# Kernel optimization log

Measured on AMD Instinct MI355X. Metric: run time of the kernel, lower is better.

## Reference

```python
import jax, jax.numpy as jnp
import numpy as np
from math import sqrt

D_MODEL = 1024
N_HEADS = 16
E = D_MODEL // N_HEADS  # d_keys = d_values = 64


def setup_inputs() -> dict:
    key = jax.random.key(0)
    ks = jax.random.split(key, 11)
    B, L, S = 2, 2048, 2048
    s = 1.0 / sqrt(D_MODEL)
    return {
        "queries": jax.random.normal(ks[0], (B, L, D_MODEL), jnp.float32),
        "keys": jax.random.normal(ks[1], (B, S, D_MODEL), jnp.float32),
        "values": jax.random.normal(ks[2], (B, S, D_MODEL), jnp.float32),
        "Wq": jax.random.normal(ks[3], (D_MODEL, D_MODEL), jnp.float32) * s,
        "bq": jnp.zeros((D_MODEL,), jnp.float32),
        "Wk": jax.random.normal(ks[4], (D_MODEL, D_MODEL), jnp.float32) * s,
        "bk": jnp.zeros((D_MODEL,), jnp.float32),
        "Wv": jax.random.normal(ks[5], (D_MODEL, D_MODEL), jnp.float32) * s,
        "bv": jnp.zeros((D_MODEL,), jnp.float32),
        "Wo": jax.random.normal(ks[6], (D_MODEL, D_MODEL), jnp.float32) * s,
        "bo": jnp.zeros((D_MODEL,), jnp.float32),
    }


def reference(queries, keys, values, Wq, bq, Wk, bk, Wv, bv, Wo, bo):
    B, L, _ = queries.shape
    S = keys.shape[1]
    H = N_HEADS
    # projections -> [B, L/S, H, E]
    q = (queries @ Wq + bq).reshape(B, L, H, E)
    k = (keys @ Wk + bk).reshape(B, S, H, E)
    v = (values @ Wv + bv).reshape(B, S, H, E)
    scale = 1.0 / sqrt(E)
    scores = jnp.einsum('blhe,bshe->bhls', q, k)  # [B,H,L,S]
    A = jax.nn.softmax(scale * scores, axis=-1)   # dropout = identity (eval)
    V = jnp.einsum('bhls,bshd->blhd', A, v)       # [B,L,H,E]
    out = V.reshape(B, L, H * E) @ Wo + bo
    return out
```

## Files before the change

### kernel.cpp

```cpp
#include <hip/hip_runtime.h>
#include <hip/hip_bf16.h>
#include <stdint.h>

#define BATCH 2
#define SEQ   2048
#define DM    1024
#define NH    16
#define EH    64
#define MROWS (BATCH*SEQ)

typedef __attribute__((ext_vector_type(8))) short  short8;
typedef __attribute__((ext_vector_type(4))) float  floatx4;
typedef __attribute__((ext_vector_type(8))) unsigned short ushort8v;
typedef __attribute__((ext_vector_type(4))) unsigned short ushort4v;

__device__ __forceinline__ unsigned short f2bf(float f) {
    return (unsigned short)((__float_as_uint(f) + 0x8000u) >> 16);
}

__device__ __forceinline__ void gload_lds16(const void* g, void* l) {
    __builtin_amdgcn_global_load_lds(
        (const __attribute__((address_space(1))) unsigned int*)g,
        (__attribute__((address_space(3))) unsigned int*)l, 16, 0, 0);
}

__global__ __launch_bounds__(256)
void transpose_w(const float* __restrict__ W0, const float* __restrict__ W1,
                 const float* __restrict__ W2, const float* __restrict__ W3,
                 unsigned short* __restrict__ T0, unsigned short* __restrict__ T1,
                 unsigned short* __restrict__ T2, unsigned short* __restrict__ T3,
                 int zbase)
{
    int z = zbase + blockIdx.z;
    const float* W = (z == 0) ? W0 : (z == 1) ? W1 : (z == 2) ? W2 : W3;
    unsigned short* T = (z == 0) ? T0 : (z == 1) ? T1 : (z == 2) ? T2 : T3;
    __shared__ float t[32][33];
    const int tid = threadIdx.x;
    const int k0 = blockIdx.y * 32, n0 = blockIdx.x * 32;
    {
        int r = tid >> 3, c4 = (tid & 7) * 4;
        float4 u = *(const float4*)&W[(size_t)(k0 + r) * DM + n0 + c4];
        t[r][c4 + 0] = u.x; t[r][c4 + 1] = u.y; t[r][c4 + 2] = u.z; t[r][c4 + 3] = u.w;
    }
    __syncthreads();
    {
        int n = tid >> 3, k4 = (tid & 7) * 4;
        ushort4v o;
        o[0] = f2bf(t[k4 + 0][n]); o[1] = f2bf(t[k4 + 1][n]);
        o[2] = f2bf(t[k4 + 2][n]); o[3] = f2bf(t[k4 + 3][n]);
        *(ushort4v*)&T[(size_t)(n0 + n) * DM + k0 + k4] = o;
    }
}

struct ProjArgs {
    const float* act[3];
    const unsigned short* wt[3];
    const float* bias[3];
    unsigned short* C[3];
    float oscale[3];
};

__global__ __launch_bounds__(256)
void proj_qkv(ProjArgs pa)
{
    const int z = blockIdx.z;
    const bool vt = (z == 2);
    const int linear = (int)(blockIdx.x + gridDim.x * blockIdx.y);
    int rb, cb;
    if (!vt) { rb = linear & 31; cb = linear >> 5; }
    else     { cb = linear & 31; rb = linear >> 5; }
    const int row0 = rb * 128, col0 = cb * 128;

    const float* act = pa.act[z];
    const unsigned short* wt = pa.wt[z];
    const int actBase = vt ? col0 : row0;
    const int wtBase  = vt ? row0 : col0;

    __shared__ unsigned short As[128 * 32];
    __shared__ unsigned short Bs[128 * 32];
    unsigned short* convDst  = vt ? Bs : As;
    unsigned short* asyncDst = vt ? As : Bs;

    const int tid = threadIdx.x;
    const int lane = tid & 63, w = tid >> 6;
    const int lane15 = lane & 15, quad = lane >> 4;

    floatx4 acc[2][8] = {};

    float4 pre[4];
    {
        const float* p0 = &act[(size_t)(actBase + (tid >> 2)) * DM + ((tid & 3) * 8)];
        const float* p1 = &act[(size_t)(actBase + ((256 + tid) >> 2)) * DM + ((tid & 3) * 8)];
        pre[0] = *(const float4*)p0; pre[1] = *(const float4*)(p0 + 4);
        pre[2] = *(const float4*)p1; pre[3] = *(const float4*)(p1 + 4);
    }

    for (int kt = 0; kt < DM; kt += 32) {
        __syncthreads();
#pragma unroll
        for (int rr = 0; rr < 2; ++rr) {
            int c = rr * 256 + tid;
            ushort8v o8;
            float4 u0 = pre[rr * 2], u1 = pre[rr * 2 + 1];
            o8[0] = f2bf(u0.x); o8[1] = f2bf(u0.y); o8[2] = f2bf(u0.z); o8[3] = f2bf(u0.w);
            o8[4] = f2bf(u1.x); o8[5] = f2bf(u1.y); o8[6] = f2bf(u1.z); o8[7] = f2bf(u1.w);
            *(ushort8v*)&convDst[(size_t)c * 8] = o8;
        }
#pragma unroll
        for (int rr = 0; rr < 2; ++rr) {
            int c = rr * 256 + w * 64 + lane;
            int row = c >> 2, kel = (c & 3) * 8;
            gload_lds16(&wt[(size_t)(wtBase + row) * DM + kt + kel],
                        (char*)asyncDst + (size_t)(rr * 256 + w * 64) * 16);
        }
        __syncthreads();

        if (kt + 32 < DM) {
            int kn = kt + 32;
            const float* p0 = &act[(size_t)(actBase + (tid >> 2)) * DM + kn + ((tid & 3) * 8)];
            const float* p1 = &act[(size_t)(actBase + ((256 + tid) >> 2)) * DM + kn + ((tid & 3) * 8)];
            pre[0] = *(const float4*)p0; pre[1] = *(const float4*)(p0 + 4);
            pre[2] = *(const float4*)p1; pre[3] = *(const float4*)(p1 + 4);
        }

        short8 af[2], bf[8];
#pragma unroll
        for (int i = 0; i < 2; ++i)
            af[i] = *(const short8*)&As[(w * 32 + i * 16 + lane15) * 32 + quad * 8];
#pragma unroll
        for (int j = 0; j < 8; ++j)
            bf[j] = *(const short8*)&Bs[(j * 16 + lane15) * 32 + quad * 8];
#pragma unroll
        for (int i = 0; i < 2; ++i)
#pragma unroll
            for (int j = 0; j < 8; ++j)
                acc[i][j] = __builtin_amdgcn_mfma_f32_16x16x32_bf16(af[i], bf[j], acc[i][j], 0, 0, 0);
    }

    const float* bias = pa.bias[z];
    const float os = pa.oscale[z];
    unsigned short* C = pa.C[z];
#pragma unroll
    for (int i = 0; i < 2; ++i) {
#pragma unroll
        for (int j = 0; j < 8; ++j) {
#pragma unroll
            for (int r = 0; r < 4; ++r) {
                int row = row0 + w * 32 + i * 16 + quad * 4 + r;
                int col = col0 + j * 16 + lane15;
                if (!vt) {
                    float v = (acc[i][j][r] + bias[col]) * os;
                    int b = row >> 11, l = row & (SEQ - 1);
                    int h = col >> 6,  e = col & (EH - 1);
                    C[((size_t)(b * NH + h) * SEQ + l) * EH + e] = f2bf(v);
                } else {
                    float v = acc[i][j][r] + bias[row];
                    int h = row >> 6,  e = row & (EH - 1);
                    int b = col >> 11, l = col & (SEQ - 1);
                    C[((size_t)(b * NH + h) * EH + e) * SEQ + l] = f2bf(v);
                }
            }
        }
    }
}

__global__ __launch_bounds__(256)
void gemm_out(const unsigned short* __restrict__ ctx,
              const unsigned short* __restrict__ WoT,
              const float* __restrict__ bo,
              float* __restrict__ out)
{
    const int linear = (int)(blockIdx.x + gridDim.x * blockIdx.y);
    const int rb = linear & 31, cb = linear >> 5;
    const int row0 = rb * 128, col0 = cb * 64;

    __shared__ unsigned short As[128 * 32];
    __shared__ unsigned short Bs[64 * 32];

    const int tid = threadIdx.x;
    const int lane = tid & 63, w = tid >> 6;
    const int lane15 = lane & 15, quad = lane >> 4;

    floatx4 acc[2][4] = {};

    for (int kt = 0; kt < DM; kt += 32) {
        __syncthreads();
#pragma unroll
        for (int rr = 0; rr < 2; ++rr) {
            int c = rr * 256 + w * 64 + lane;
            int row = c >> 2, kel = (c & 3) * 8;
            gload_lds16(&ctx[(size_t)(row0 + row) * DM + kt + kel],
                        (char*)As + (size_t)(rr * 256 + w * 64) * 16);
        }
        {
            int c = w * 64 + lane;
            int row = c >> 2, kel = (c & 3) * 8;
            gload_lds16(&WoT[(size_t)(col0 + row) * DM + kt + kel],
                        (char*)Bs + (size_t)(w * 64) * 16);
        }
        __syncthreads();

        short8 af[2], bf[4];
#pragma unroll
        for (int i = 0; i < 2; ++i)
            af[i] = *(const short8*)&As[(w * 32 + i * 16 + lane15) * 32 + quad * 8];
#pragma unroll
        for (int j = 0; j < 4; ++j)
            bf[j] = *(const short8*)&Bs[(j * 16 + lane15) * 32 + quad * 8];
#pragma unroll
        for (int i = 0; i < 2; ++i)
#pragma unroll
            for (int j = 0; j < 4; ++j)
                acc[i][j] = __builtin_amdgcn_mfma_f32_16x16x32_bf16(af[i], bf[j], acc[i][j], 0, 0, 0);
    }

#pragma unroll
    for (int i = 0; i < 2; ++i)
#pragma unroll
        for (int j = 0; j < 4; ++j)
#pragma unroll
            for (int r = 0; r < 4; ++r) {
                int row = row0 + w * 32 + i * 16 + quad * 4 + r;
                int col = col0 + j * 16 + lane15;
                out[(size_t)row * DM + col] = acc[i][j][r] + bo[col];
            }
}

__device__ __forceinline__ void stage_kv(const unsigned short* __restrict__ Kp,
                                         const unsigned short* __restrict__ Vp,
                                         int st, unsigned short* ksb, unsigned short* vsb,
                                         int w, int lane)
{
#pragma unroll
    for (int rr = 0; rr < 2; ++rr) {
        int p = rr * 256 + w * 64 + lane;
        int row = p >> 3;
        int gch = (p & 7) ^ (row & 7);
        gload_lds16(&Kp[(size_t)(st + row) * EH + gch * 8],
                    ksb + (size_t)(rr * 256 + w * 64) * 8);
        gload_lds16(&Vp[(size_t)row * SEQ + st + gch * 8],
                    vsb + (size_t)(rr * 256 + w * 64) * 8);
    }
}

__global__ __launch_bounds__(256)
void attn_mfma(const unsigned short* __restrict__ Qh,
               const unsigned short* __restrict__ Kh,
               const unsigned short* __restrict__ Vt,
               unsigned short* __restrict__ ctx)
{
    __shared__ unsigned short Ks[2][64 * 64];
    __shared__ unsigned short Vs[2][64 * 64];
    __shared__ unsigned short Ps[128][72];

    const int tid = threadIdx.x;
    const int lane = tid & 63, w = tid >> 6;
    const int lane15 = lane & 15, quad = lane >> 4;

    const int linear = (int)(blockIdx.x + 16 * (blockIdx.y + 16 * blockIdx.z));
    const int bhid = linear & 31;
    const int qt = linear >> 5;
    const int h = bhid & 15, b = bhid >> 4;

    const size_t bh = (size_t)(b * NH + h);
    const unsigned short* Kp = Kh + bh * SEQ * EH;
    const unsigned short* Vp = Vt + bh * EH * SEQ;

    short8 qf[2][2];
    {
        const unsigned short* Qp =
            Qh + (bh * SEQ + (size_t)qt * 128 + w * 32 + lane15) * EH;
#pragma unroll
        for (int ks = 0; ks < 2; ++ks) {
            qf[0][ks] = *(const short8*)(Qp + ks * 32 + quad * 8);
            qf[1][ks] = *(const short8*)(Qp + 16 * EH + ks * 32 + quad * 8);
        }
    }
    short8 ones;
#pragma unroll
    for (int i = 0; i < 8; ++i) ones[i] = (short)0x3F80;

    floatx4 o[2][4] = {};
    floatx4 lacc[2] = {};

    stage_kv(Kp, Vp, 0, Ks[0], Vs[0], w, lane);
    __syncthreads();
    int cur = 0;

    for (int st = 0; st < SEQ; st += 64) {
        int nxt = cur ^ 1;
        if (st + 64 < SEQ)
            stage_kv(Kp, Vp, st + 64, Ks[nxt], Vs[nxt], w, lane);
        const unsigned short* ksb = Ks[cur];
        const unsigned short* vsb = Vs[cur];

        floatx4 sacc[4][2] = {};
#pragma unroll
        for (int ts = 0; ts < 4; ++ts) {
#pragma unroll
            for (int ks = 0; ks < 2; ++ks) {
                short8 kf = *(const short8*)&ksb[((ts * 16 + lane15) << 6) +
                                                 ((((ks << 2) + quad) ^ (lane15 & 7)) << 3)];
                sacc[ts][0] = __builtin_amdgcn_mfma_f32_16x16x32_bf16(kf, qf[0][ks], sacc[ts][0], 0, 0, 0);
                sacc[ts][1] = __builtin_amdgcn_mfma_f32_16x16x32_bf16(kf, qf[1][ks], sacc[ts][1], 0, 0, 0);
            }
        }

#pragma unroll
        for (int ts = 0; ts < 4; ++ts)
#pragma unroll
            for (int nq = 0; nq < 2; ++nq) {
                unsigned int u0 = __float_as_uint(__builtin_amdgcn_exp2f(sacc[ts][nq][0])) + 0x8000u;
                unsigned int u1 = __float_as_uint(__builtin_amdgcn_exp2f(sacc[ts][nq][1])) + 0x8000u;
                unsigned int u2 = __float_as_uint(__builtin_amdgcn_exp2f(sacc[ts][nq][2])) + 0x8000u;
                unsigned int u3 = __float_as_uint(__builtin_amdgcn_exp2f(sacc[ts][nq][3])) + 0x8000u;
                uint2 pk;
                pk.x = (u0 >> 16) | (u1 & 0xFFFF0000u);
                pk.y = (u2 >> 16) | (u3 & 0xFFFF0000u);
                *(uint2*)&Ps[w * 32 + nq * 16 + lane15][ts * 16 + quad * 4] = pk;
            }

#pragma unroll
        for (int ks = 0; ks < 2; ++ks) {
            short8 pf[2];
#pragma unroll
            for (int mt = 0; mt < 2; ++mt) {
                pf[mt] = *(const short8*)&Ps[w * 32 + mt * 16 + lane15][ks * 32 + quad * 8];
                lacc[mt] = __builtin_amdgcn_mfma_f32_16x16x32_bf16(pf[mt], ones, lacc[mt], 0, 0, 0);
            }
#pragma unroll
            for (int t2 = 0; t2 < 4; ++t2) {
                short8 vf = *(const short8*)&vsb[((t2 * 16 + lane15) << 6) +
                                                 ((((ks << 2) + quad) ^ (lane15 & 7)) << 3)];
                o[0][t2] = __builtin_amdgcn_mfma_f32_16x16x32_bf16(pf[0], vf, o[0][t2], 0, 0, 0);
                o[1][t2] = __builtin_amdgcn_mfma_f32_16x16x32_bf16(pf[1], vf, o[1][t2], 0, 0, 0);
            }
        }
        __syncthreads();
        cur = nxt;
    }

#pragma unroll
    for (int mt = 0; mt < 2; ++mt) {
        float inv[4];
#pragma unroll
        for (int r = 0; r < 4; ++r) inv[r] = 1.0f / lacc[mt][r];
#pragma unroll
        for (int t2 = 0; t2 < 4; ++t2)
#pragma unroll
            for (int r = 0; r < 4; ++r) {
                int q = qt * 128 + w * 32 + mt * 16 + quad * 4 + r;
                int col = h * EH + t2 * 16 + lane15;
                ctx[((size_t)(b * SEQ + q)) * DM + col] = f2bf(o[mt][t2][r] * inv[r]);
            }
    }
}

extern "C" void kernel_launch(void* const* d_in, const int* in_sizes, int n_in,
                              void* d_out, int out_size, void* d_ws, size_t ws_size,
                              hipStream_t stream)
{
    const float* queries = (const float*)d_in[0];
    const float* keys    = (const float*)d_in[1];
    const float* values  = (const float*)d_in[2];
    const float* Wq = (const float*)d_in[3];
    const float* bq = (const float*)d_in[4];
    const float* Wk = (const float*)d_in[5];
    const float* bk = (const float*)d_in[6];
    const float* Wv = (const float*)d_in[7];
    const float* bv = (const float*)d_in[8];
    const float* Wo = (const float*)d_in[9];
    const float* bo = (const float*)d_in[10];
    float* out = (float*)d_out;

    unsigned short* ws = (unsigned short*)d_ws;
    const size_t MAT = (size_t)MROWS * DM;
    const size_t WSZ = (size_t)DM * DM;
    unsigned short* Qhp = ws;
    unsigned short* Khp = ws + MAT;
    unsigned short* Vtp = ws + 2 * MAT;
    unsigned short* ctx = ws + 3 * MAT;
    unsigned short* WqT = ctx;
    unsigned short* WkT = ctx + WSZ;
    unsigned short* WvT = ctx + 2 * WSZ;
    unsigned short* WoT = ws;

    const float qscale = 0.125f * 1.44269504088896f;

    transpose_w<<<dim3(DM / 32, DM / 32, 3), 256, 0, stream>>>(
        Wq, Wk, Wv, Wo, WqT, WkT, WvT, WoT, 0);

    ProjArgs pa;
    pa.act[0] = queries; pa.act[1] = keys; pa.act[2] = values;
    pa.wt[0] = WqT;      pa.wt[1] = WkT;   pa.wt[2] = WvT;
    pa.bias[0] = bq;     pa.bias[1] = bk;  pa.bias[2] = bv;
    pa.C[0] = Qhp;       pa.C[1] = Khp;    pa.C[2] = Vtp;
    pa.oscale[0] = qscale; pa.oscale[1] = 1.f; pa.oscale[2] = 1.f;
    proj_qkv<<<dim3(8, 32, 3), 256, 0, stream>>>(pa);

    attn_mfma<<<dim3(SEQ / 128, NH, BATCH), 256, 0, stream>>>(Qhp, Khp, Vtp, ctx);

    transpose_w<<<dim3(DM / 32, DM / 32, 1), 256, 0, stream>>>(
        Wq, Wk, Wv, Wo, WqT, WkT, WvT, WoT, 3);

    gemm_out<<<dim3(16, 32), 256, 0, stream>>>(ctx, WoT, bo, out);
}
```

Before: 227.4 us.

## Double-buffer LDS in projection GEMMs with XOR swizzle and 2x2 warp tiling

Both projection and output GEMMs now use two LDS buffers, prefetching the next K tile while computing the current one, so each iteration needs one barrier instead of two. LDS chunk positions are XOR-swizzled on store and load to reduce bank conflicts on the fragment reads. In the QKV projection, warps are rearranged into a 2x2 grid of 64x64 tiles, which cuts redundant B-fragment LDS reads. This doubles LDS use per block and may lower occupancy.

```diff
diff --git a/kernel.cpp b/kernel.cpp
--- a/kernel.cpp
+++ b/kernel.cpp
@@ -76,78 +76,94 @@
     const int actBase = vt ? col0 : row0;
     const int wtBase  = vt ? row0 : col0;
 
-    __shared__ unsigned short As[128 * 32];
-    __shared__ unsigned short Bs[128 * 32];
-    unsigned short* convDst  = vt ? Bs : As;
-    unsigned short* asyncDst = vt ? As : Bs;
+    __shared__ unsigned short As[2][128 * 32];
+    __shared__ unsigned short Bs[2][128 * 32];
+    unsigned short* conv[2] = { vt ? Bs[0] : As[0], vt ? Bs[1] : As[1] };
+    unsigned short* wdst[2] = { vt ? As[0] : Bs[0], vt ? As[1] : Bs[1] };
 
     const int tid = threadIdx.x;
     const int lane = tid & 63, w = tid >> 6;
     const int lane15 = lane & 15, quad = lane >> 4;
-
-    floatx4 acc[2][8] = {};
+    const int wr = (w >> 1) * 64, wc = (w & 1) * 64;
+
+    floatx4 acc[4][4] = {};
 
     float4 pre[4];
-    {
-        const float* p0 = &act[(size_t)(actBase + (tid >> 2)) * DM + ((tid & 3) * 8)];
-        const float* p1 = &act[(size_t)(actBase + ((256 + tid) >> 2)) * DM + ((tid & 3) * 8)];
+    const int arow = tid >> 2;
+    const int acol = (tid & 3) * 8;
+
+    auto loadPre = [&](int kt) {
+        const float* p0 = &act[(size_t)(actBase + arow) * DM + kt + acol];
+        const float* p1 = &act[(size_t)(actBase + 64 + arow) * DM + kt + acol];
         pre[0] = *(const float4*)p0; pre[1] = *(const float4*)(p0 + 4);
         pre[2] = *(const float4*)p1; pre[3] = *(const float4*)(p1 + 4);
-    }
-
-    for (int kt = 0; kt < DM; kt += 32) {
-        __syncthreads();
+    };
+    auto cvtStore = [&](unsigned short* dst) {
 #pragma unroll
         for (int rr = 0; rr < 2; ++rr) {
-            int c = rr * 256 + tid;
+            int row = rr * 64 + arow;
+            int cp = (tid & 3) ^ ((row >> 1) & 3);
+            float4 u0 = pre[rr * 2], u1 = pre[rr * 2 + 1];
             ushort8v o8;
-            float4 u0 = pre[rr * 2], u1 = pre[rr * 2 + 1];
             o8[0] = f2bf(u0.x); o8[1] = f2bf(u0.y); o8[2] = f2bf(u0.z); o8[3] = f2bf(u0.w);
             o8[4] = f2bf(u1.x); o8[5] = f2bf(u1.y); o8[6] = f2bf(u1.z); o8[7] = f2bf(u1.w);
-            *(ushort8v*)&convDst[(size_t)c * 8] = o8;
-        }
+            *(ushort8v*)&dst[(size_t)(row * 4 + cp) * 8] = o8;
+        }
+    };
+    auto stageW = [&](int kt, unsigned short* dst) {
 #pragma unroll
         for (int rr = 0; rr < 2; ++rr) {
-            int c = rr * 256 + w * 64 + lane;
-            int row = c >> 2, kel = (c & 3) * 8;
-            gload_lds16(&wt[(size_t)(wtBase + row) * DM + kt + kel],
-                        (char*)asyncDst + (size_t)(rr * 256 + w * 64) * 16);
-        }
+            int p = rr * 256 + w * 64 + lane;
+            int row = p >> 2;
+            int gch = (p & 3) ^ ((row >> 1) & 3);
+            gload_lds16(&wt[(size_t)(wtBase + row) * DM + kt + gch * 8],
+                        (char*)dst + (size_t)(rr * 256 + w * 64) * 16);
+        }
+    };
+
+    loadPre(0);
+    stageW(0, wdst[0]);
+    cvtStore(conv[0]);
+    loadPre(32);
+    __syncthreads();
+
+    const int sw = (lane15 >> 1) & 3;
+    for (int kt = 0; kt < DM; kt += 32) {
+        const int cur = (kt >> 5) & 1, nxt = cur ^ 1;
+        if (kt + 32 < DM) {
+            stageW(kt + 32, wdst[nxt]);
+            cvtStore(conv[nxt]);
+            if (kt + 64 < DM) loadPre(kt + 64);
+        }
+
+        const unsigned short* as = As[cur];
+        const unsigned short* bs = Bs[cur];
+        short8 af[4], bf[4];
+#pragma unroll
+        for (int i = 0; i < 4; ++i)
+            af[i] = *(const short8*)&as[(size_t)(wr + i * 16 + lane15) * 32 + ((quad ^ sw) << 3)];
+#pragma unroll
+        for (int j = 0; j < 4; ++j)
+            bf[j] = *(const short8*)&bs[(size_t)(wc + j * 16 + lane15) * 32 + ((quad ^ sw) << 3)];
+#pragma unroll
+        for (int i = 0; i < 4; ++i)
+#pragma unroll
+            for (int j = 0; j < 4; ++j)
+                acc[i][j] = __builtin_amdgcn_mfma_f32_16x16x32_bf16(af[i], bf[j], acc[i][j], 0, 0, 0);
         __syncthreads();
-
-        if (kt + 32 < DM) {
-            int kn = kt + 32;
-            const float* p0 = &act[(size_t)(actBase + (tid >> 2)) * DM + kn + ((tid & 3) * 8)];
-            const float* p1 = &act[(size_t)(actBase + ((256 + tid) >> 2)) * DM + kn + ((tid & 3) * 8)];
-            pre[0] = *(const float4*)p0; pre[1] = *(const float4*)(p0 + 4);
-            pre[2] = *(const float4*)p1; pre[3] = *(const float4*)(p1 + 4);
-        }
-
-        short8 af[2], bf[8];
-#pragma unroll
-        for (int i = 0; i < 2; ++i)
-            af[i] = *(const short8*)&As[(w * 32 + i * 16 + lane15) * 32 + quad * 8];
-#pragma unroll
-        for (int j = 0; j < 8; ++j)
-            bf[j] = *(const short8*)&Bs[(j * 16 + lane15) * 32 + quad * 8];
-#pragma unroll
-        for (int i = 0; i < 2; ++i)
-#pragma unroll
-            for (int j = 0; j < 8; ++j)
-                acc[i][j] = __builtin_amdgcn_mfma_f32_16x16x32_bf16(af[i], bf[j], acc[i][j], 0, 0, 0);
     }
 
     const float* bias = pa.bias[z];
     const float os = pa.oscale[z];
     unsigned short* C = pa.C[z];
 #pragma unroll
-    for (int i = 0; i < 2; ++i) {
-#pragma unroll
-        for (int j = 0; j < 8; ++j) {
+    for (int i = 0; i < 4; ++i) {
+#pragma unroll
+        for (int j = 0; j < 4; ++j) {
 #pragma unroll
             for (int r = 0; r < 4; ++r) {
-                int row = row0 + w * 32 + i * 16 + quad * 4 + r;
-                int col = col0 + j * 16 + lane15;
+                int row = row0 + wr + i * 16 + quad * 4 + r;
+                int col = col0 + wc + j * 16 + lane15;
                 if (!vt) {
                     float v = (acc[i][j][r] + bias[col]) * os;
                     int b = row >> 11, l = row & (SEQ - 1);
@@ -174,8 +190,8 @@
     const int rb = linear & 31, cb = linear >> 5;
     const int row0 = rb * 128, col0 = cb * 64;
 
-    __shared__ unsigned short As[128 * 32];
-    __shared__ unsigned short Bs[64 * 32];
+    __shared__ unsigned short As[2][128 * 32];
+    __shared__ unsigned short Bs[2][64 * 32];
 
     const int tid = threadIdx.x;
     const int lane = tid & 63, w = tid >> 6;
@@ -183,35 +199,51 @@
 
     floatx4 acc[2][4] = {};
 
+    auto stageA = [&](int kt, unsigned short* dst) {
+#pragma unroll
+        for (int rr = 0; rr < 2; ++rr) {
+            int p = rr * 256 + w * 64 + lane;
+            int row = p >> 2;
+            int gch = (p & 3) ^ ((row >> 1) & 3);
+            gload_lds16(&ctx[(size_t)(row0 + row) * DM + kt + gch * 8],
+                        (char*)dst + (size_t)(rr * 256 + w * 64) * 16);
+        }
+    };
+    auto stageB = [&](int kt, unsigned short* dst) {
+        int p = w * 64 + lane;
+        int row = p >> 2;
+        int gch = (p & 3) ^ ((row >> 1) & 3);
+        gload_lds16(&WoT[(size_t)(col0 + row) * DM + kt + gch * 8],
+                    (char*)dst + (size_t)(w * 64) * 16);
+    };
+
+    stageA(0, As[0]);
+    stageB(0, Bs[0]);
+    __syncthreads();
+
+    const int sw = (lane15 >> 1) & 3;
     for (int kt = 0; kt < DM; kt += 32) {
-        __syncthreads();
-#pragma unroll
-        for (int rr = 0; rr < 2; ++rr) {
-            int c = rr * 256 + w * 64 + lane;
-            int row = c >> 2, kel = (c & 3) * 8;
-            gload_lds16(&ctx[(size_t)(row0 + row) * DM + kt + kel],
-                        (char*)As + (size_t)(rr * 256 + w * 64) * 16);
-        }
-        {
-            int c = w * 64 + lane;
-            int row = c >> 2, kel = (c & 3) * 8;
-            gload_lds16(&WoT[(size_t)(col0 + row) * DM + kt + kel],
-                        (char*)Bs + (size_t)(w * 64) * 16);
-        }
-        __syncthreads();
-
+        const int cur = (kt >> 5) & 1, nxt = cur ^ 1;
+        if (kt + 32 < DM) {
+            stageA(kt + 32, As[nxt]);
+            stageB(kt + 32, Bs[nxt]);
+        }
+
+        const unsigned short* as = As[cur];
+        const unsigned short* bs = Bs[cur];
         short8 af[2], bf[4];
 #pragma unroll
         for (int i = 0; i < 2; ++i)
-            af[i] = *(const short8*)&As[(w * 32 + i * 16 + lane15) * 32 + quad * 8];
+            af[i] = *(const short8*)&as[(size_t)(w * 32 + i * 16 + lane15) * 32 + ((quad ^ sw) << 3)];
 #pragma unroll
         for (int j = 0; j < 4; ++j)
-            bf[j] = *(const short8*)&Bs[(j * 16 + lane15) * 32 + quad * 8];
+            bf[j] = *(const short8*)&bs[(size_t)(j * 16 + lane15) * 32 + ((quad ^ sw) << 3)];
 #pragma unroll
         for (int i = 0; i < 2; ++i)
 #pragma unroll
             for (int j = 0; j < 4; ++j)
                 acc[i][j] = __builtin_amdgcn_mfma_f32_16x16x32_bf16(af[i], bf[j], acc[i][j], 0, 0, 0);
+        __syncthreads();
     }
 
 #pragma unroll
```

Result: slower. 274.3 us (+20.6%).

## Shrink GEMM tiles to 64-row blocks, use 2x2 warp grid, and XOR-swizzle LDS

Applied to the files above, without the earlier changes.

The QKV projection and output GEMM now use 64-row tiles instead of 128-row ones, which doubles the number of blocks. Warps are arranged in a 2x2 grid over the tile, so each warp holds fewer accumulators. LDS stores and reads are XOR-swizzled by 16-byte chunk to avoid bank conflicts when fragments are loaded. The aim is better occupancy and CU fill and fewer LDS conflicts, at the cost of more redundant global traffic per output element because each tile reuses less data.

```diff
diff --git a/kernel.cpp b/kernel.cpp
--- a/kernel.cpp
+++ b/kernel.cpp
@@ -67,73 +67,91 @@
     const bool vt = (z == 2);
     const int linear = (int)(blockIdx.x + gridDim.x * blockIdx.y);
     int rb, cb;
-    if (!vt) { rb = linear & 31; cb = linear >> 5; }
+    if (!vt) { rb = linear & 63; cb = linear >> 6; }
     else     { cb = linear & 31; rb = linear >> 5; }
-    const int row0 = rb * 128, col0 = cb * 128;
+    const int row0 = rb * 64, col0 = cb * 128;
 
     const float* act = pa.act[z];
     const unsigned short* wt = pa.wt[z];
     const int actBase = vt ? col0 : row0;
     const int wtBase  = vt ? row0 : col0;
 
-    __shared__ unsigned short As[128 * 32];
+    __shared__ unsigned short As[64 * 32];
     __shared__ unsigned short Bs[128 * 32];
-    unsigned short* convDst  = vt ? Bs : As;
-    unsigned short* asyncDst = vt ? As : Bs;
+    unsigned short* conv = vt ? Bs : As;
+    unsigned short* wdst = vt ? As : Bs;
 
     const int tid = threadIdx.x;
     const int lane = tid & 63, w = tid >> 6;
     const int lane15 = lane & 15, quad = lane >> 4;
-
-    floatx4 acc[2][8] = {};
+    const int wr = (w >> 1) * 32, wc = (w & 1) * 64;
+
+    floatx4 acc[2][4] = {};
 
     float4 pre[4];
-    {
-        const float* p0 = &act[(size_t)(actBase + (tid >> 2)) * DM + ((tid & 3) * 8)];
-        const float* p1 = &act[(size_t)(actBase + ((256 + tid) >> 2)) * DM + ((tid & 3) * 8)];
+    const int arow = tid >> 2;
+    const int acol = (tid & 3) * 8;
+
+    auto loadPre = [&](int kt) {
+        const float* p0 = &act[(size_t)(actBase + arow) * DM + kt + acol];
         pre[0] = *(const float4*)p0; pre[1] = *(const float4*)(p0 + 4);
-        pre[2] = *(const float4*)p1; pre[3] = *(const float4*)(p1 + 4);
-    }
-
+        if (vt) {
+            const float* p1 = &act[(size_t)(actBase + 64 + arow) * DM + kt + acol];
+            pre[2] = *(const float4*)p1; pre[3] = *(const float4*)(p1 + 4);
+        }
+    };
+    auto cvtStore = [&]() {
+        int cp = (tid & 3) ^ ((arow >> 1) & 3);
+        {
+            float4 u0 = pre[0], u1 = pre[1];
+            ushort8v o8;
+            o8[0] = f2bf(u0.x); o8[1] = f2bf(u0.y); o8[2] = f2bf(u0.z); o8[3] = f2bf(u0.w);
+            o8[4] = f2bf(u1.x); o8[5] = f2bf(u1.y); o8[6] = f2bf(u1.z); o8[7] = f2bf(u1.w);
+            *(ushort8v*)&conv[(size_t)(arow * 4 + cp) * 8] = o8;
+        }
+        if (vt) {
+            float4 u0 = pre[2], u1 = pre[3];
+            ushort8v o8;
+            o8[0] = f2bf(u0.x); o8[1] = f2bf(u0.y); o8[2] = f2bf(u0.z); o8[3] = f2bf(u0.w);
+            o8[4] = f2bf(u1.x); o8[5] = f2bf(u1.y); o8[6] = f2bf(u1.z); o8[7] = f2bf(u1.w);
+            *(ushort8v*)&conv[(size_t)((64 + arow) * 4 + cp) * 8] = o8;
+        }
+    };
+    auto stageW = [&](int kt) {
+        {
+            int p = w * 64 + lane;
+            int row = p >> 2, gch = (p & 3) ^ ((row >> 1) & 3);
+            gload_lds16(&wt[(size_t)(wtBase + row) * DM + kt + gch * 8],
+                        (char*)wdst + (size_t)(w * 64) * 16);
+        }
+        if (!vt) {
+            int p = 256 + w * 64 + lane;
+            int row = p >> 2, gch = (p & 3) ^ ((row >> 1) & 3);
+            gload_lds16(&wt[(size_t)(wtBase + row) * DM + kt + gch * 8],
+                        (char*)wdst + (size_t)(256 + w * 64) * 16);
+        }
+    };
+
+    loadPre(0);
+    const int sw = (lane15 >> 1) & 3;
     for (int kt = 0; kt < DM; kt += 32) {
         __syncthreads();
-#pragma unroll
-        for (int rr = 0; rr < 2; ++rr) {
-            int c = rr * 256 + tid;
-            ushort8v o8;
-            float4 u0 = pre[rr * 2], u1 = pre[rr * 2 + 1];
-            o8[0] = f2bf(u0.x); o8[1] = f2bf(u0.y); o8[2] = f2bf(u0.z); o8[3] = f2bf(u0.w);
-            o8[4] = f2bf(u1.x); o8[5] = f2bf(u1.y); o8[6] = f2bf(u1.z); o8[7] = f2bf(u1.w);
-            *(ushort8v*)&convDst[(size_t)c * 8] = o8;
-        }
-#pragma unroll
-        for (int rr = 0; rr < 2; ++rr) {
-            int c = rr * 256 + w * 64 + lane;
-            int row = c >> 2, kel = (c & 3) * 8;
-            gload_lds16(&wt[(size_t)(wtBase + row) * DM + kt + kel],
-                        (char*)asyncDst + (size_t)(rr * 256 + w * 64) * 16);
-        }
+        cvtStore();
+        stageW(kt);
         __syncthreads();
-
-        if (kt + 32 < DM) {
-            int kn = kt + 32;
-            const float* p0 = &act[(size_t)(actBase + (tid >> 2)) * DM + kn + ((tid & 3) * 8)];
-            const float* p1 = &act[(size_t)(actBase + ((256 + tid) >> 2)) * DM + kn + ((tid & 3) * 8)];
-            pre[0] = *(const float4*)p0; pre[1] = *(const float4*)(p0 + 4);
-            pre[2] = *(const float4*)p1; pre[3] = *(const float4*)(p1 + 4);
-        }
-
-        short8 af[2], bf[8];
+        if (kt + 32 < DM) loadPre(kt + 32);
+
+        short8 af[2], bf[4];
 #pragma unroll
         for (int i = 0; i < 2; ++i)
-            af[i] = *(const short8*)&As[(w * 32 + i * 16 + lane15) * 32 + quad * 8];
-#pragma unroll
-        for (int j = 0; j < 8; ++j)
-            bf[j] = *(const short8*)&Bs[(j * 16 + lane15) * 32 + quad * 8];
+            af[i] = *(const short8*)&As[((size_t)(wr + i * 16 + lane15) * 4 + (quad ^ sw)) * 8];
+#pragma unroll
+        for (int j = 0; j < 4; ++j)
+            bf[j] = *(const short8*)&Bs[((size_t)(wc + j * 16 + lane15) * 4 + (quad ^ sw)) * 8];
 #pragma unroll
         for (int i = 0; i < 2; ++i)
 #pragma unroll
-            for (int j = 0; j < 8; ++j)
+            for (int j = 0; j < 4; ++j)
                 acc[i][j] = __builtin_amdgcn_mfma_f32_16x16x32_bf16(af[i], bf[j], acc[i][j], 0, 0, 0);
     }
 
@@ -143,11 +161,11 @@
 #pragma unroll
     for (int i = 0; i < 2; ++i) {
 #pragma unroll
-        for (int j = 0; j < 8; ++j) {
+        for (int j = 0; j < 4; ++j) {
 #pragma unroll
             for (int r = 0; r < 4; ++r) {
-                int row = row0 + w * 32 + i * 16 + quad * 4 + r;
-                int col = col0 + j * 16 + lane15;
+                int row = row0 + wr + i * 16 + quad * 4 + r;
+                int col = col0 + wc + j * 16 + lane15;
                 if (!vt) {
                     float v = (acc[i][j][r] + bias[col]) * os;
                     int b = row >> 11, l = row & (SEQ - 1);
@@ -171,57 +189,55 @@
               float* __restrict__ out)
 {
     const int linear = (int)(blockIdx.x + gridDim.x * blockIdx.y);
-    const int rb = linear & 31, cb = linear >> 5;
-    const int row0 = rb * 128, col0 = cb * 64;
-
-    __shared__ unsigned short As[128 * 32];
+    const int rb = linear & 63, cb = linear >> 6;
+    const int row0 = rb * 64, col0 = cb * 64;
+
+    __shared__ unsigned short As[64 * 32];
     __shared__ unsigned short Bs[64 * 32];
 
     const int tid = threadIdx.x;
     const int lane = tid & 63, w = tid >> 6;
     const int lane15 = lane & 15, quad = lane >> 4;
-
-    floatx4 acc[2][4] = {};
-
+    const int wr = (w >> 1) * 32, wc = (w & 1) * 32;
+
+    floatx4 acc[2][2] = {};
+
+    auto stage = [&](const unsigned short* src, int base, int kt, unsigned short* dst) {
+        int p = w * 64 + lane;
+        int row = p >> 2, gch = (p & 3) ^ ((row >> 1) & 3);
+        gload_lds16(&src[(size_t)(base + row) * DM + kt + gch * 8],
+                    (char*)dst + (size_t)(w * 64) * 16);
+    };
+
+    const int sw = (lane15 >> 1) & 3;
     for (int kt = 0; kt < DM; kt += 32) {
         __syncthreads();
-#pragma unroll
-        for (int rr = 0; rr < 2; ++rr) {
-            int c = rr * 256 + w * 64 + lane;
-            int row = c >> 2, kel = (c & 3) * 8;
-            gload_lds16(&ctx[(size_t)(row0 + row) * DM + kt + kel],
-                        (char*)As + (size_t)(rr * 256 + w * 64) * 16);
-        }
-        {
-            int c = w * 64 + lane;
-            int row = c >> 2, kel = (c & 3) * 8;
-            gload_lds16(&WoT[(size_t)(col0 + row) * DM + kt + kel],
-                        (char*)Bs + (size_t)(w * 64) * 16);
-        }
+        stage(ctx, row0, kt, As);
+        stage(WoT, col0, kt, Bs);
         __syncthreads();
 
-        short8 af[2], bf[4];
+        short8 af[2], bf[2];
 #pragma unroll
         for (int i = 0; i < 2; ++i)
-            af[i] = *(const short8*)&As[(w * 32 + i * 16 + lane15) * 32 + quad * 8];
-#pragma unroll
-        for (int j = 0; j < 4; ++j)
-            bf[j] = *(const short8*)&Bs[(j * 16 + lane15) * 32 + quad * 8];
+            af[i] = *(const short8*)&As[((size_t)(wr + i * 16 + lane15) * 4 + (quad ^ sw)) * 8];
+#pragma unroll
+        for (int j = 0; j < 2; ++j)
+            bf[j] = *(const short8*)&Bs[((size_t)(wc + j * 16 + lane15) * 4 + (quad ^ sw)) * 8];
 #pragma unroll
         for (int i = 0; i < 2; ++i)
 #pragma unroll
-            for (int j = 0; j < 4; ++j)
+            for (int j = 0; j < 2; ++j)
                 acc[i][j] = __builtin_amdgcn_mfma_f32_16x16x32_bf16(af[i], bf[j], acc[i][j], 0, 0, 0);
     }
 
 #pragma unroll
     for (int i = 0; i < 2; ++i)
 #pragma unroll
-        for (int j = 0; j < 4; ++j)
+        for (int j = 0; j < 2; ++j)
 #pragma unroll
             for (int r = 0; r < 4; ++r) {
-                int row = row0 + w * 32 + i * 16 + quad * 4 + r;
-                int col = col0 + j * 16 + lane15;
+                int row = row0 + wr + i * 16 + quad * 4 + r;
+                int col = col0 + wc + j * 16 + lane15;
                 out[(size_t)row * DM + col] = acc[i][j][r] + bo[col];
             }
 }
@@ -396,12 +412,12 @@
     pa.bias[0] = bq;     pa.bias[1] = bk;  pa.bias[2] = bv;
     pa.C[0] = Qhp;       pa.C[1] = Khp;    pa.C[2] = Vtp;
     pa.oscale[0] = qscale; pa.oscale[1] = 1.f; pa.oscale[2] = 1.f;
-    proj_qkv<<<dim3(8, 32, 3), 256, 0, stream>>>(pa);
+    proj_qkv<<<dim3(8, 64, 3), 256, 0, stream>>>(pa);
 
     attn_mfma<<<dim3(SEQ / 128, NH, BATCH), 256, 0, stream>>>(Qhp, Khp, Vtp, ctx);
 
     transpose_w<<<dim3(DM / 32, DM / 32, 1), 256, 0, stream>>>(
         Wq, Wk, Wv, Wo, WqT, WkT, WvT, WoT, 3);
 
-    gemm_out<<<dim3(16, 32), 256, 0, stream>>>(ctx, WoT, bo, out);
-}
+    gemm_out<<<dim3(16, 64), 256, 0, stream>>>(ctx, WoT, bo, out);
+}
```

Measured after the change: 255.9 us. 12.5% more time.

## Swizzle GEMM LDS tiles and halve attention query tile per block

Applied to the files above, without the earlier changes.

The projection and output GEMMs now store their 32-wide bf16 K-chunks in LDS with an XOR swizzle on the 16-byte chunk index, and the MFMA fragment reads apply the matching swizzle. This is meant to remove LDS bank conflicts on the fragment loads. Separately, the attention kernel now handles 64 queries per block instead of 128, 16 per wave, which doubles the grid and shrinks registers and the P buffer to raise occupancy and parallelism. The cost is that each block reloads K/V tiles for half as many queries, doubling K/V traffic.

```diff
diff --git a/kernel.cpp b/kernel.cpp
--- a/kernel.cpp
+++ b/kernel.cpp
@@ -95,22 +95,26 @@
         pre[2] = *(const float4*)p1; pre[3] = *(const float4*)(p1 + 4);
     }
 
+    const int cp = (tid & 3) ^ (((tid >> 2) >> 1) & 3);
+    const int sw = (lane15 >> 1) & 3;
+
     for (int kt = 0; kt < DM; kt += 32) {
         __syncthreads();
 #pragma unroll
         for (int rr = 0; rr < 2; ++rr) {
-            int c = rr * 256 + tid;
+            int row = rr * 64 + (tid >> 2);
             ushort8v o8;
             float4 u0 = pre[rr * 2], u1 = pre[rr * 2 + 1];
             o8[0] = f2bf(u0.x); o8[1] = f2bf(u0.y); o8[2] = f2bf(u0.z); o8[3] = f2bf(u0.w);
             o8[4] = f2bf(u1.x); o8[5] = f2bf(u1.y); o8[6] = f2bf(u1.z); o8[7] = f2bf(u1.w);
-            *(ushort8v*)&convDst[(size_t)c * 8] = o8;
+            *(ushort8v*)&convDst[(size_t)(row * 4 + cp) * 8] = o8;
         }
 #pragma unroll
         for (int rr = 0; rr < 2; ++rr) {
             int c = rr * 256 + w * 64 + lane;
-            int row = c >> 2, kel = (c & 3) * 8;
-            gload_lds16(&wt[(size_t)(wtBase + row) * DM + kt + kel],
+            int row = c >> 2;
+            int gch = (c & 3) ^ ((row >> 1) & 3);
+            gload_lds16(&wt[(size_t)(wtBase + row) * DM + kt + gch * 8],
                         (char*)asyncDst + (size_t)(rr * 256 + w * 64) * 16);
         }
         __syncthreads();
@@ -126,10 +130,10 @@
         short8 af[2], bf[8];
 #pragma unroll
         for (int i = 0; i < 2; ++i)
-            af[i] = *(const short8*)&As[(w * 32 + i * 16 + lane15) * 32 + quad * 8];
+            af[i] = *(const short8*)&As[(w * 32 + i * 16 + lane15) * 32 + ((quad ^ sw) << 3)];
 #pragma unroll
         for (int j = 0; j < 8; ++j)
-            bf[j] = *(const short8*)&Bs[(j * 16 + lane15) * 32 + quad * 8];
+            bf[j] = *(const short8*)&Bs[(j * 16 + lane15) * 32 + ((quad ^ sw) << 3)];
 #pragma unroll
         for (int i = 0; i < 2; ++i)
 #pragma unroll
@@ -180,6 +184,7 @@
     const int tid = threadIdx.x;
     const int lane = tid & 63, w = tid >> 6;
     const int lane15 = lane & 15, quad = lane >> 4;
+    const int sw = (lane15 >> 1) & 3;
 
     floatx4 acc[2][4] = {};
 
@@ -188,14 +193,16 @@
 #pragma unroll
         for (int rr = 0; rr < 2; ++rr) {
             int c = rr * 256 + w * 64 + lane;
-            int row = c >> 2, kel = (c & 3) * 8;
-            gload_lds16(&ctx[(size_t)(row0 + row) * DM + kt + kel],
+            int row = c >> 2;
+            int gch = (c & 3) ^ ((row >> 1) & 3);
+            gload_lds16(&ctx[(size_t)(row0 + row) * DM + kt + gch * 8],
                         (char*)As + (size_t)(rr * 256 + w * 64) * 16);
         }
         {
             int c = w * 64 + lane;
-            int row = c >> 2, kel = (c & 3) * 8;
-            gload_lds16(&WoT[(size_t)(col0 + row) * DM + kt + kel],
+            int row = c >> 2;
+            int gch = (c & 3) ^ ((row >> 1) & 3);
+            gload_lds16(&WoT[(size_t)(col0 + row) * DM + kt + gch * 8],
                         (char*)Bs + (size_t)(w * 64) * 16);
         }
         __syncthreads();
@@ -203,10 +210,10 @@
         short8 af[2], bf[4];
 #pragma unroll
         for (int i = 0; i < 2; ++i)
-            af[i] = *(const short8*)&As[(w * 32 + i * 16 + lane15) * 32 + quad * 8];
+            af[i] = *(const short8*)&As[(w * 32 + i * 16 + lane15) * 32 + ((quad ^ sw) << 3)];
 #pragma unroll
         for (int j = 0; j < 4; ++j)
-            bf[j] = *(const short8*)&Bs[(j * 16 + lane15) * 32 + quad * 8];
+            bf[j] = *(const short8*)&Bs[(j * 16 + lane15) * 32 + ((quad ^ sw) << 3)];
 #pragma unroll
         for (int i = 0; i < 2; ++i)
 #pragma unroll
@@ -251,13 +258,13 @@
 {
     __shared__ unsigned short Ks[2][64 * 64];
     __shared__ unsigned short Vs[2][64 * 64];
-    __shared__ unsigned short Ps[128][72];
+    __shared__ unsigned short Ps[64][72];
 
     const int tid = threadIdx.x;
     const int lane = tid & 63, w = tid >> 6;
     const int lane15 = lane & 15, quad = lane >> 4;
 
-    const int linear = (int)(blockIdx.x + 16 * (blockIdx.y + 16 * blockIdx.z));
+    const int linear = (int)(blockIdx.x + 32 * (blockIdx.y + 16 * blockIdx.z));
     const int bhid = linear & 31;
     const int qt = linear >> 5;
     const int h = bhid & 15, b = bhid >> 4;
@@ -266,22 +273,20 @@
     const unsigned short* Kp = Kh + bh * SEQ * EH;
     const unsigned short* Vp = Vt + bh * EH * SEQ;
 
-    short8 qf[2][2];
+    short8 qf[2];
     {
         const unsigned short* Qp =
-            Qh + (bh * SEQ + (size_t)qt * 128 + w * 32 + lane15) * EH;
-#pragma unroll
-        for (int ks = 0; ks < 2; ++ks) {
-            qf[0][ks] = *(const short8*)(Qp + ks * 32 + quad * 8);
-            qf[1][ks] = *(const short8*)(Qp + 16 * EH + ks * 32 + quad * 8);
-        }
+            Qh + (bh * SEQ + (size_t)qt * 64 + w * 16 + lane15) * EH;
+#pragma unroll
+        for (int ks = 0; ks < 2; ++ks)
+            qf[ks] = *(const short8*)(Qp + ks * 32 + quad * 8);
     }
     short8 ones;
 #pragma unroll
     for (int i = 0; i < 8; ++i) ones[i] = (short)0x3F80;
 
-    floatx4 o[2][4] = {};
-    floatx4 lacc[2] = {};
+    floatx4 o[4] = {};
+    floatx4 lacc = {};
 
     stage_kv(Kp, Vp, 0, Ks[0], Vs[0], w, lane);
     __syncthreads();
@@ -294,64 +299,55 @@
         const unsigned short* ksb = Ks[cur];
         const unsigned short* vsb = Vs[cur];
 
-        floatx4 sacc[4][2] = {};
+        floatx4 sacc[4] = {};
 #pragma unroll
         for (int ts = 0; ts < 4; ++ts) {
 #pragma unroll
             for (int ks = 0; ks < 2; ++ks) {
                 short8 kf = *(const short8*)&ksb[((ts * 16 + lane15) << 6) +
                                                  ((((ks << 2) + quad) ^ (lane15 & 7)) << 3)];
-                sacc[ts][0] = __builtin_amdgcn_mfma_f32_16x16x32_bf16(kf, qf[0][ks], sacc[ts][0], 0, 0, 0);
-                sacc[ts][1] = __builtin_amdgcn_mfma_f32_16x16x32_bf16(kf, qf[1][ks], sacc[ts][1], 0, 0, 0);
+                sacc[ts] = __builtin_amdgcn_mfma_f32_16x16x32_bf16(kf, qf[ks], sacc[ts], 0, 0, 0);
             }
         }
 
 #pragma unroll
-        for (int ts = 0; ts < 4; ++ts)
-#pragma unroll
-            for (int nq = 0; nq < 2; ++nq) {
-                unsigned int u0 = __float_as_uint(__builtin_amdgcn_exp2f(sacc[ts][nq][0])) + 0x8000u;
-                unsigned int u1 = __float_as_uint(__builtin_amdgcn_exp2f(sacc[ts][nq][1])) + 0x8000u;
-                unsigned int u2 = __float_as_uint(__builtin_amdgcn_exp2f(sacc[ts][nq][2])) + 0x8000u;
-                unsigned int u3 = __float_as_uint(__builtin_amdgcn_exp2f(sacc[ts][nq][3])) + 0x8000u;
-                uint2 pk;
-                pk.x = (u0 >> 16) | (u1 & 0xFFFF0000u);
-                pk.y = (u2 >> 16) | (u3 & 0xFFFF0000u);
-                *(uint2*)&Ps[w * 32 + nq * 16 + lane15][ts * 16 + quad * 4] = pk;
-            }
+        for (int ts = 0; ts < 4; ++ts) {
+            unsigned int u0 = __float_as_uint(__builtin_amdgcn_exp2f(sacc[ts][0])) + 0x8000u;
+            unsigned int u1 = __float_as_uint(__builtin_amdgcn_exp2f(sacc[ts][1])) + 0x8000u;
+            unsigned int u2 = __float_as_uint(__builtin_amdgcn_exp2f(sacc[ts][2])) + 0x8000u;
+            unsigned int u3 = __float_as_uint(__builtin_amdgcn_exp2f(sacc[ts][3])) + 0x8000u;
+            uint2 pk;
+            pk.x = (u0 >> 16) | (u1 & 0xFFFF0000u);
+            pk.y = (u2 >> 16) | (u3 & 0xFFFF0000u);
+            *(uint2*)&Ps[w * 16 + lane15][ts * 16 + quad * 4] = pk;
+        }
 
 #pragma unroll
         for (int ks = 0; ks < 2; ++ks) {
-            short8 pf[2];
-#pragma unroll
-            for (int mt = 0; mt < 2; ++mt) {
-                pf[mt] = *(const short8*)&Ps[w * 32 + mt * 16 + lane15][ks * 32 + quad * 8];
-                lacc[mt] = __builtin_amdgcn_mfma_f32_16x16x32_bf16(pf[mt], ones, lacc[mt], 0, 0, 0);
-            }
+            short8 pf = *(const short8*)&Ps[w * 16 + lane15][ks * 32 + quad * 8];
+            lacc = __builtin_amdgcn_mfma_f32_16x16x32_bf16(pf, ones, lacc, 0, 0, 0);
 #pragma unroll
             for (int t2 = 0; t2 < 4; ++t2) {
                 short8 vf = *(const short8*)&vsb[((t2 * 16 + lane15) << 6) +
                                                  ((((ks << 2) + quad) ^ (lane15 & 7)) << 3)];
-                o[0][t2] = __builtin_amdgcn_mfma_f32_16x16x32_bf16(pf[0], vf, o[0][t2], 0, 0, 0);
-                o[1][t2] = __builtin_amdgcn_mfma_f32_16x16x32_bf16(pf[1], vf, o[1][t2], 0, 0, 0);
+                o[t2] = __builtin_amdgcn_mfma_f32_16x16x32_bf16(pf, vf, o[t2], 0, 0, 0);
             }
         }
         __syncthreads();
         cur = nxt;
     }
 
-#pragma unroll
-    for (int mt = 0; mt < 2; ++mt) {
+    {
         float inv[4];
 #pragma unroll
-        for (int r = 0; r < 4; ++r) inv[r] = 1.0f / lacc[mt][r];
+        for (int r = 0; r < 4; ++r) inv[r] = 1.0f / lacc[r];
 #pragma unroll
         for (int t2 = 0; t2 < 4; ++t2)
 #pragma unroll
             for (int r = 0; r < 4; ++r) {
-                int q = qt * 128 + w * 32 + mt * 16 + quad * 4 + r;
+                int q = qt * 64 + w * 16 + quad * 4 + r;
                 int col = h * EH + t2 * 16 + lane15;
-                ctx[((size_t)(b * SEQ + q)) * DM + col] = f2bf(o[mt][t2][r] * inv[r]);
+                ctx[((size_t)(b * SEQ + q)) * DM + col] = f2bf(o[t2][r] * inv[r]);
             }
     }
 }
@@ -398,7 +394,7 @@
     pa.oscale[0] = qscale; pa.oscale[1] = 1.f; pa.oscale[2] = 1.f;
     proj_qkv<<<dim3(8, 32, 3), 256, 0, stream>>>(pa);
 
-    attn_mfma<<<dim3(SEQ / 128, NH, BATCH), 256, 0, stream>>>(Qhp, Khp, Vtp, ctx);
+    attn_mfma<<<dim3(SEQ / 64, NH, BATCH), 256, 0, stream>>>(Qhp, Khp, Vtp, ctx);
 
     transpose_w<<<dim3(DM / 32, DM / 32, 1), 256, 0, stream>>>(
         Wq, Wk, Wv, Wo, WqT, WkT, WvT, WoT, 3);
```

Result: slower. 255.1 us (+12.2%).
